# Optimization experiments

Measured on AMD Instinct MI355X. Metric: run time of the kernel, lower is better.

## Reference

```python
import jax, jax.numpy as jnp
import numpy as np
import math

B, S, H, NH, K = 1, 4096, 1024, 16, 32
HD = H // NH


def setup_inputs() -> dict:
    key = jax.random.key(0)
    ks = jax.random.split(key, 8)
    x = jax.random.normal(ks[0], (B, S, H), dtype=jnp.float32)
    # per-query top-K indices; make them causal (idx[q] <= q) so every row has >=1 valid key
    idx_raw = jax.random.randint(ks[1], (S, K), 0, S)
    idx = idx_raw % (jnp.arange(S)[:, None] + 1)
    valid = jnp.ones((S, K), dtype=bool)
    geo_bias = jax.random.normal(ks[2], (NH, S, K), dtype=jnp.float32)
    scale = 1.0 / math.sqrt(H)
    Wq = jax.random.normal(ks[3], (H, H), dtype=jnp.float32) * scale
    Wk = jax.random.normal(ks[4], (H, H), dtype=jnp.float32) * scale
    Wv = jax.random.normal(ks[5], (H, H), dtype=jnp.float32) * scale
    Wo = jax.random.normal(ks[6], (H, H), dtype=jnp.float32) * scale
    bo = jnp.zeros((H,), dtype=jnp.float32)
    return {"x": x, "idx": idx, "valid": valid, "geo_bias": geo_bias,
            "Wq": Wq, "Wk": Wk, "Wv": Wv, "Wo": Wo, "bo": bo}


def reference(x, idx, valid, geo_bias, Wq, Wk, Wv, Wo, bo):
    b, s, h = x.shape
    nh = geo_bias.shape[0]
    hd = h // nh
    kk = idx.shape[1]
    # projections -> [b, nh, s, hd]
    def proj(W):
        return (x @ W).reshape(b, s, nh, hd).transpose(0, 2, 1, 3)
    q, k, v = proj(Wq), proj(Wk), proj(Wv)
    # gather per-query selected keys/values: [b, nh, s, K, hd]
    k_sel = k[:, :, idx]
    v_sel = v[:, :, idx]
    # scores via elementwise mult + reduce over head_dim
    logits = jnp.einsum('bhsd,bhskd->bhsk', q, k_sel) / math.sqrt(hd)
    logits = logits + geo_bias[None]
    mask = valid & (idx <= jnp.arange(s)[:, None])  # [s, K]
    logits = jnp.where(mask[None, None], logits, jnp.float32(-1e30))
    attn = jax.nn.softmax(logits, axis=-1)
    out = jnp.einsum('bhsk,bhskd->bhsd', attn, v_sel)
    out = out.transpose(0, 2, 1, 3).reshape(b, s, h)
    return out @ Wo + bo
```

## Files before the change

### kernel.cpp

```cpp
#include <hip/hip_runtime.h>
#include <hip/hip_bf16.h>
#include <stdint.h>

typedef unsigned short u16;
typedef __attribute__((ext_vector_type(8))) short bf16x8;
typedef __attribute__((ext_vector_type(4))) float f32x4;
typedef __attribute__((ext_vector_type(2))) float f32x2;

typedef const __attribute__((address_space(1))) unsigned int* gptr_t;
typedef __attribute__((address_space(3))) unsigned int* lptr_t;

__device__ __forceinline__ float bf2f(u16 v) {
    unsigned int u = ((unsigned int)v) << 16;
    float f;
    __builtin_memcpy(&f, &u, 4);
    return f;
}
__device__ __forceinline__ u16 f2bf(float f) {
    unsigned int u;
    __builtin_memcpy(&u, &f, 4);
    u += 0x7FFFu + ((u >> 16) & 1u);
    return (u16)(u >> 16);
}
__device__ __forceinline__ float bflo(unsigned int u) {
    unsigned int x = u << 16; float f; __builtin_memcpy(&f, &x, 4); return f;
}
__device__ __forceinline__ float bfhi(unsigned int u) {
    unsigned int x = u & 0xFFFF0000u; float f; __builtin_memcpy(&f, &x, 4); return f;
}
__device__ __forceinline__ f32x2 upk(unsigned int u) {
    return (f32x2){bflo(u), bfhi(u)};
}

#define BM 128
#define BN 128
#define BK 32

template <typename OUTT>
__global__ __launch_bounds__(256) void gemm_bt(const u16* __restrict__ A,
                                               const u16* __restrict__ Bt,
                                               OUTT* __restrict__ C,
                                               const float* __restrict__ bias,
                                               int M, int N, int K) {
    __shared__ u16 As[BM * BK];
    __shared__ u16 Bs[BN * BK];

    const int t    = threadIdx.x;
    const int lane = t & 63;
    const int wave = t >> 6;
    const int wm   = (wave >> 1) * 64;
    const int wn   = (wave & 1) * 64;
    const int m0   = blockIdx.y * BM;
    const int n0   = blockIdx.x * BN;

    const int row  = t >> 2;
    const int kcol = (t & 3) * 8;

    const int quad = lane >> 4;
    const int l16  = lane & 15;

    f32x4 acc[4][4];
#pragma unroll
    for (int i = 0; i < 4; i++)
#pragma unroll
        for (int j = 0; j < 4; j++) acc[i][j] = (f32x4){0.f, 0.f, 0.f, 0.f};

    for (int k0 = 0; k0 < K; k0 += BK) {
        const u16* ga  = A  + (size_t)(m0 + row) * K + k0 + kcol;
        const u16* ga2 = A  + (size_t)(m0 + 64 + row) * K + k0 + kcol;
        const u16* gb  = Bt + (size_t)(n0 + row) * K + k0 + kcol;
        const u16* gb2 = Bt + (size_t)(n0 + 64 + row) * K + k0 + kcol;
        __builtin_amdgcn_global_load_lds((gptr_t)ga,  (lptr_t)(&As[t * 8]),        16, 0, 0);
        __builtin_amdgcn_global_load_lds((gptr_t)ga2, (lptr_t)(&As[2048 + t * 8]), 16, 0, 0);
        __builtin_amdgcn_global_load_lds((gptr_t)gb,  (lptr_t)(&Bs[t * 8]),        16, 0, 0);
        __builtin_amdgcn_global_load_lds((gptr_t)gb2, (lptr_t)(&Bs[2048 + t * 8]), 16, 0, 0);
        __syncthreads();

        bf16x8 af[4], bfg[4];
#pragma unroll
        for (int i = 0; i < 4; i++)
            af[i] = *(const bf16x8*)&As[(wm + i * 16 + l16) * BK + quad * 8];
#pragma unroll
        for (int j = 0; j < 4; j++)
            bfg[j] = *(const bf16x8*)&Bs[(wn + j * 16 + l16) * BK + quad * 8];

#pragma unroll
        for (int i = 0; i < 4; i++)
#pragma unroll
            for (int j = 0; j < 4; j++)
                acc[i][j] = __builtin_amdgcn_mfma_f32_16x16x32_bf16(af[i], bfg[j], acc[i][j], 0, 0, 0);
        __syncthreads();
    }

#pragma unroll
    for (int j = 0; j < 4; j++) {
        const int n  = n0 + wn + j * 16 + l16;
        const float bv = bias ? bias[n] : 0.f;
#pragma unroll
        for (int i = 0; i < 4; i++) {
            const int mbase = m0 + wm + i * 16 + quad * 4;
#pragma unroll
            for (int r = 0; r < 4; r++) {
                const float v = acc[i][j][r] + bv;
                if constexpr (sizeof(OUTT) == 2)
                    C[(size_t)(mbase + r) * N + n] = (OUTT)f2bf(v);
                else
                    C[(size_t)(mbase + r) * N + n] = (OUTT)v;
            }
        }
    }
}

__global__ __launch_bounds__(256) void cvt_f32_bf16(const float* __restrict__ src,
                                                    u16* __restrict__ dst, int n4) {
    const int i = blockIdx.x * 256 + threadIdx.x;
    if (i >= n4) return;
    const float4 v = ((const float4*)src)[i];
    u16 o[4] = {f2bf(v.x), f2bf(v.y), f2bf(v.z), f2bf(v.w)};
    *(uint64_t*)&dst[i * 4] = *(uint64_t*)o;
}

__global__ __launch_bounds__(256) void transpose4_k(const float* __restrict__ W0,
                                                    const float* __restrict__ W1,
                                                    const float* __restrict__ W2,
                                                    const float* __restrict__ W3,
                                                    u16* __restrict__ Dqkv,
                                                    u16* __restrict__ Do) {
    __shared__ u16 tile[32][33];
    const int z = blockIdx.z;
    const float* src = (z == 0) ? W0 : (z == 1) ? W1 : (z == 2) ? W2 : W3;
    u16* dst = (z < 3) ? (Dqkv + (size_t)z * 1024 * 1024) : Do;
    const int tx = threadIdx.x & 31;
    const int ty = threadIdx.x >> 5;
    const int c0 = blockIdx.x * 32;
    const int r0 = blockIdx.y * 32;
#pragma unroll
    for (int i = 0; i < 32; i += 8)
        tile[ty + i][tx] = f2bf(src[(size_t)(r0 + ty + i) * 1024 + c0 + tx]);
    __syncthreads();
#pragma unroll
    for (int i = 0; i < 32; i += 8)
        dst[(size_t)(c0 + ty + i) * 1024 + r0 + tx] = tile[tx][ty + i];
}

__global__ __launch_bounds__(256) void attn_k(const u16* __restrict__ QKV,
                                              const int* __restrict__ idx,
                                              const float* __restrict__ geo,
                                              u16* __restrict__ AO) {
    __shared__ uint4 k_lds[4 * 512];
    __shared__ uint4 q_lds[4 * 16];
    __shared__ float w_lds[4 * 64];

    const int t    = threadIdx.x;
    const int lane = t & 63;
    const int wave = t >> 6;
    const int gid  = blockIdx.x * 4 + wave;
    const int hp   = gid & 7;
    const int s    = gid >> 3;
    const int h0   = hp * 2;
    const int hsel = lane >> 5;
    const int kk   = lane & 31;

    const char* qb = (const char*)QKV;

    if (lane < 16)
        q_lds[wave * 16 + lane] =
            *(const uint4*)(qb + (size_t)s * 6144 + h0 * 128 + lane * 16);

    const int j    = idx[s * 32 + kk];
    const int joff = j * 6144;

    const int lg = lane >> 3;
    const int c8 = lane & 7;
    const int pw = c8 ^ lg;
#pragma unroll
    for (int i = 0; i < 8; i++) {
        const int rh   = i * 8 + lg;
        const int jm   = __shfl(j, rh & 31);
        const int hoff = (h0 + (i >> 2)) * 128;
        const uint4 kv = *(const uint4*)(qb + (size_t)(unsigned)(jm * 6144) + 2048 + hoff + c8 * 16);
        k_lds[wave * 512 + rh * 8 + pw] = kv;
    }

    f32x2 d2 = (f32x2){0.f, 0.f};
#pragma unroll
    for (int c = 0; c < 8; c++) {
        const uint4 kc = k_lds[wave * 512 + lane * 8 + (c ^ c8)];
        const uint4 qc = q_lds[wave * 16 + hsel * 8 + c];
        d2 += upk(qc.x) * upk(kc.x);
        d2 += upk(qc.y) * upk(kc.y);
        d2 += upk(qc.z) * upk(kc.z);
        d2 += upk(qc.w) * upk(kc.w);
    }
    const float dot = d2.x + d2.y;

    float lg2 = dot * 0.125f + geo[((size_t)(h0 + hsel) * 4096 + s) * 32 + kk];
    if (j > s) lg2 = -1e30f;

    float mx = lg2;
    mx = fmaxf(mx, __shfl_xor(mx, 16));
    mx = fmaxf(mx, __shfl_xor(mx, 8));
    mx = fmaxf(mx, __shfl_xor(mx, 4));
    mx = fmaxf(mx, __shfl_xor(mx, 2));
    mx = fmaxf(mx, __shfl_xor(mx, 1));
    const float p = __expf(lg2 - mx);
    float sum = p;
    sum += __shfl_xor(sum, 16);
    sum += __shfl_xor(sum, 8);
    sum += __shfl_xor(sum, 4);
    sum += __shfl_xor(sum, 2);
    sum += __shfl_xor(sum, 1);
    const float w = p / sum;
    w_lds[wave * 64 + lane] = w;

    const int vbyte = 4096 + h0 * 128 + 4 * lane;
    f32x2 av = (f32x2){0.f, 0.f};
#pragma unroll
    for (int q = 0; q < 32; q++) {
        const int soff = __builtin_amdgcn_readlane(joff, q);
        const float wq = w_lds[wave * 64 + (lane & 32) + q];
        const unsigned int vv = *(const unsigned int*)(qb + (size_t)(unsigned)soff + vbyte);
        av += wq * upk(vv);
    }
    const unsigned int packed = (unsigned int)f2bf(av.x) | ((unsigned int)f2bf(av.y) << 16);
    *(unsigned int*)&AO[(size_t)s * 1024 + h0 * 64 + 2 * lane] = packed;
}

extern "C" void kernel_launch(void* const* d_in, const int* in_sizes, int n_in,
                              void* d_out, int out_size, void* d_ws, size_t ws_size,
                              hipStream_t stream) {
    const float* x   = (const float*)d_in[0];
    const int*   idx = (const int*)d_in[1];
    const float* geo = (const float*)d_in[3];
    const float* Wq  = (const float*)d_in[4];
    const float* Wk  = (const float*)d_in[5];
    const float* Wv  = (const float*)d_in[6];
    const float* Wo  = (const float*)d_in[7];
    const float* bo  = (const float*)d_in[8];
    float* out = (float*)d_out;

    u16* x_bf   = (u16*)d_ws;
    u16* wt_qkv = x_bf + (size_t)4096 * 1024;
    u16* wt_o   = wt_qkv + (size_t)3 * 1024 * 1024;
    u16* qkv    = wt_o + (size_t)1024 * 1024;
    u16* ao     = qkv + (size_t)4096 * 3072;

    const dim3 tb(256);
    cvt_f32_bf16<<<dim3(4096), tb, 0, stream>>>(x, x_bf, 4096 * 1024 / 4);
    transpose4_k<<<dim3(32, 32, 4), tb, 0, stream>>>(Wq, Wk, Wv, Wo, wt_qkv, wt_o);

    gemm_bt<u16><<<dim3(3072 / BN, 4096 / BM), tb, 0, stream>>>(x_bf, wt_qkv, qkv, nullptr,
                                                                4096, 3072, 1024);
    attn_k<<<dim3(4096 * 8 / 4), tb, 0, stream>>>(qkv, idx, geo, ao);
    gemm_bt<float><<<dim3(1024 / BN, 4096 / BM), tb, 0, stream>>>(ao, wt_o, out, bo,
                                                                  4096, 1024, 1024);
}
```

Before: 202.3 us.

## Merge prep kernels and compute attention scores from registers with shuffle reductions

```diff
diff --git a/kernel.cpp b/kernel.cpp
--- a/kernel.cpp
+++ b/kernel.cpp
@@ -111,29 +111,32 @@
     }
 }
 
-__global__ __launch_bounds__(256) void cvt_f32_bf16(const float* __restrict__ src,
-                                                    u16* __restrict__ dst, int n4) {
-    const int i = blockIdx.x * 256 + threadIdx.x;
-    if (i >= n4) return;
-    const float4 v = ((const float4*)src)[i];
-    u16 o[4] = {f2bf(v.x), f2bf(v.y), f2bf(v.z), f2bf(v.w)};
-    *(uint64_t*)&dst[i * 4] = *(uint64_t*)o;
-}
-
-__global__ __launch_bounds__(256) void transpose4_k(const float* __restrict__ W0,
-                                                    const float* __restrict__ W1,
-                                                    const float* __restrict__ W2,
-                                                    const float* __restrict__ W3,
-                                                    u16* __restrict__ Dqkv,
-                                                    u16* __restrict__ Do) {
+__global__ __launch_bounds__(256) void prep_k(const float* __restrict__ x,
+                                              const float* __restrict__ W0,
+                                              const float* __restrict__ W1,
+                                              const float* __restrict__ W2,
+                                              const float* __restrict__ W3,
+                                              u16* __restrict__ x_bf,
+                                              u16* __restrict__ Dqkv,
+                                              u16* __restrict__ Do) {
+    const int b = blockIdx.x;
+    if (b < 4096) {
+        const int i = b * 256 + threadIdx.x;
+        const float4 v = ((const float4*)x)[i];
+        u16 o[4] = {f2bf(v.x), f2bf(v.y), f2bf(v.z), f2bf(v.w)};
+        *(uint64_t*)&x_bf[i * 4] = *(uint64_t*)o;
+        return;
+    }
     __shared__ u16 tile[32][33];
-    const int z = blockIdx.z;
+    const int bb  = b - 4096;
+    const int z   = bb >> 10;
+    const int t10 = bb & 1023;
+    const int c0  = (t10 & 31) * 32;
+    const int r0  = (t10 >> 5) * 32;
     const float* src = (z == 0) ? W0 : (z == 1) ? W1 : (z == 2) ? W2 : W3;
     u16* dst = (z < 3) ? (Dqkv + (size_t)z * 1024 * 1024) : Do;
     const int tx = threadIdx.x & 31;
     const int ty = threadIdx.x >> 5;
-    const int c0 = blockIdx.x * 32;
-    const int r0 = blockIdx.y * 32;
 #pragma unroll
     for (int i = 0; i < 32; i += 8)
         tile[ty + i][tx] = f2bf(src[(size_t)(r0 + ty + i) * 1024 + c0 + tx]);
@@ -147,8 +150,7 @@
                                               const int* __restrict__ idx,
                                               const float* __restrict__ geo,
                                               u16* __restrict__ AO) {
-    __shared__ uint4 k_lds[4 * 512];
-    __shared__ uint4 q_lds[4 * 16];
+    __shared__ float dot_lds[4 * 64];
     __shared__ float w_lds[4 * 64];
 
     const int t    = threadIdx.x;
@@ -160,41 +162,46 @@
     const int h0   = hp * 2;
     const int hsel = lane >> 5;
     const int kk   = lane & 31;
+    const int g    = lane >> 3;
+    const int c8   = lane & 7;
 
     const char* qb = (const char*)QKV;
-
-    if (lane < 16)
-        q_lds[wave * 16 + lane] =
-            *(const uint4*)(qb + (size_t)s * 6144 + h0 * 128 + lane * 16);
 
     const int j    = idx[s * 32 + kk];
     const int joff = j * 6144;
 
-    const int lg = lane >> 3;
-    const int c8 = lane & 7;
-    const int pw = c8 ^ lg;
+    const uint4 qA = *(const uint4*)(qb + (size_t)s * 6144 + h0 * 128 + c8 * 16);
+    const uint4 qB = *(const uint4*)(qb + (size_t)s * 6144 + h0 * 128 + 128 + c8 * 16);
+    const f32x2 qa0 = upk(qA.x), qa1 = upk(qA.y), qa2 = upk(qA.z), qa3 = upk(qA.w);
+    const f32x2 qb0 = upk(qB.x), qb1 = upk(qB.y), qb2 = upk(qB.z), qb3 = upk(qB.w);
+
 #pragma unroll
     for (int i = 0; i < 8; i++) {
-        const int rh   = i * 8 + lg;
-        const int jm   = __shfl(j, rh & 31);
-        const int hoff = (h0 + (i >> 2)) * 128;
-        const uint4 kv = *(const uint4*)(qb + (size_t)(unsigned)(jm * 6144) + 2048 + hoff + c8 * 16);
-        k_lds[wave * 512 + rh * 8 + pw] = kv;
-    }
-
-    f32x2 d2 = (f32x2){0.f, 0.f};
-#pragma unroll
-    for (int c = 0; c < 8; c++) {
-        const uint4 kc = k_lds[wave * 512 + lane * 8 + (c ^ c8)];
-        const uint4 qc = q_lds[wave * 16 + hsel * 8 + c];
-        d2 += upk(qc.x) * upk(kc.x);
-        d2 += upk(qc.y) * upk(kc.y);
-        d2 += upk(qc.z) * upk(kc.z);
-        d2 += upk(qc.w) * upk(kc.w);
-    }
-    const float dot = d2.x + d2.y;
-
-    float lg2 = dot * 0.125f + geo[((size_t)(h0 + hsel) * 4096 + s) * 32 + kk];
+        const int rh = i * 8 + g;
+        const int jm = __shfl(j, rh & 31);
+        const uint4 kv = *(const uint4*)(qb + (size_t)(unsigned)(jm * 6144) + 2048 +
+                                         (h0 + (i >> 2)) * 128 + c8 * 16);
+        f32x2 d2;
+        if (i < 4) {
+            d2  = upk(kv.x) * qa0;
+            d2 += upk(kv.y) * qa1;
+            d2 += upk(kv.z) * qa2;
+            d2 += upk(kv.w) * qa3;
+        } else {
+            d2  = upk(kv.x) * qb0;
+            d2 += upk(kv.y) * qb1;
+            d2 += upk(kv.z) * qb2;
+            d2 += upk(kv.w) * qb3;
+        }
+        float d = d2.x + d2.y;
+        d += __shfl_xor(d, 1);
+        d += __shfl_xor(d, 2);
+        d += __shfl_xor(d, 4);
+        if (c8 == 0) dot_lds[wave * 64 + rh] = d;
+    }
+
+    float lg2 = dot_lds[wave * 64 + lane] * 0.125f +
+                geo[((size_t)(h0 + hsel) * 4096 + s) * 32 + kk];
     if (j > s) lg2 = -1e30f;
 
     float mx = lg2;
@@ -213,13 +220,13 @@
     const float w = p / sum;
     w_lds[wave * 64 + lane] = w;
 
-    const int vbyte = 4096 + h0 * 128 + 4 * lane;
+    const int vofs = 4096 + h0 * 128 + 4 * lane;
     f32x2 av = (f32x2){0.f, 0.f};
 #pragma unroll
     for (int q = 0; q < 32; q++) {
         const int soff = __builtin_amdgcn_readlane(joff, q);
         const float wq = w_lds[wave * 64 + (lane & 32) + q];
-        const unsigned int vv = *(const unsigned int*)(qb + (size_t)(unsigned)soff + vbyte);
+        const unsigned int vv = *(const unsigned int*)(qb + (size_t)(unsigned)soff + vofs);
         av += wq * upk(vv);
     }
     const unsigned int packed = (unsigned int)f2bf(av.x) | ((unsigned int)f2bf(av.y) << 16);
@@ -246,8 +253,7 @@
     u16* ao     = qkv + (size_t)4096 * 3072;
 
     const dim3 tb(256);
-    cvt_f32_bf16<<<dim3(4096), tb, 0, stream>>>(x, x_bf, 4096 * 1024 / 4);
-    transpose4_k<<<dim3(32, 32, 4), tb, 0, stream>>>(Wq, Wk, Wv, Wo, wt_qkv, wt_o);
+    prep_k<<<dim3(8192), tb, 0, stream>>>(x, Wq, Wk, Wv, Wo, x_bf, wt_qkv, wt_o);
 
     gemm_bt<u16><<<dim3(3072 / BN, 4096 / BM), tb, 0, stream>>>(x_bf, wt_qkv, qkv, nullptr,
                                                                 4096, 3072, 1024);
```

Measured after the change: 198.4 us. Within noise of the previous version (-1.9%).
